# Optimization experiments

Measured on AMD Instinct MI355X. Metric: run time of the kernel, lower is better.

The kernel has to match this reference:

```python
import jax, jax.numpy as jnp
import numpy as np

VOCAB = 250002
UNUSED = np.array([0, 2, 1, 3])  # cls, eos, pad, unk token ids for XLM-R tokenizer
TEMP = 0.02
H = 1024


def _normalize(x, axis=-1):
    n = jnp.sqrt(jnp.sum(x * x, axis=axis, keepdims=True))
    return x / jnp.maximum(n, 1e-12)


def _sparse_embedding(hidden, ids, sparse_w, sparse_b):
    # token_weights = relu(Linear(H,1)(hidden)) -> [B, L]
    tw = jax.nn.relu(jnp.einsum('blh,h->bl', hidden, sparse_w) + sparse_b)
    B = hidden.shape[0]
    # torch: scatter into [B, L, V] then max over L; since tw >= 0 and base is 0,
    # this equals a scatter-max into [B, V] (avoids the huge [B,L,V] intermediate).
    emb = jnp.zeros((B, VOCAB), tw.dtype)
    emb = emb.at[jnp.arange(B)[:, None], ids].max(tw)
    emb = emb.at[:, UNUSED].set(0.0)
    return emb


def _colbert_embedding(hidden, mask, colbert_w, colbert_b):
    # Linear on tokens 1: (drop CLS), mask, then L2-normalize
    v = jnp.einsum('blh,dh->bld', hidden[:, 1:], colbert_w) + colbert_b
    v = v * mask[:, 1:, None]
    return _normalize(v)


def setup_inputs() -> dict:
    key = jax.random.key(0)
    ks = jax.random.split(key, 8)
    return {
        'q_hidden': jax.random.normal(ks[0], (8, 128, H), jnp.float32),
        'p_hidden': jax.random.normal(ks[1], (64, 512, H), jnp.float32),
        'q_mask': jnp.ones((8, 128), jnp.float32),
        'p_mask': jnp.ones((64, 512), jnp.float32),
        'q_ids': jax.random.randint(ks[2], (8, 128), 0, VOCAB),
        'p_ids': jax.random.randint(ks[3], (64, 512), 0, VOCAB),
        'colbert_w': jax.random.normal(ks[4], (H, H), jnp.float32) * 0.02,
        'colbert_b': jnp.zeros((H,), jnp.float32),
        'sparse_w': jax.random.normal(ks[5], (H,), jnp.float32) * 0.02,
        'sparse_b': jnp.zeros((), jnp.float32),
    }


def reference(q_hidden, p_hidden, q_mask, p_mask, q_ids, p_ids,
              colbert_w, colbert_b, sparse_w, sparse_b):
    # dense: cls pooling + normalize
    q_dense = _normalize(q_hidden[:, 0])
    p_dense = _normalize(p_hidden[:, 0])
    dense_scores = (q_dense @ p_dense.T) / TEMP  # [Bq, Bp]

    # sparse: relu-weighted vocab scatter-max
    q_sparse = _sparse_embedding(q_hidden, q_ids, sparse_w, sparse_b)
    p_sparse = _sparse_embedding(p_hidden, p_ids, sparse_w, sparse_b)
    sparse_scores = (q_sparse @ p_sparse.T) / TEMP  # [Bq, Bp]

    # colbert: late-interaction maxsim
    q_col = _colbert_embedding(q_hidden, q_mask, colbert_w, colbert_b)  # [Bq, Lq-1, H]
    p_col = _colbert_embedding(p_hidden, p_mask, colbert_w, colbert_b)  # [Bp, Lp-1, H]
    token_scores = jnp.einsum('qin,pjn->qipj', q_col, p_col)  # [Bq, Lq-1, Bp, Lp-1]
    colbert_scores = token_scores.max(-1).sum(1)
    colbert_scores = colbert_scores / q_mask[:, 1:].sum(-1, keepdims=True)
    colbert_scores = colbert_scores / TEMP  # [Bq, Bp]

    return dense_scores, sparse_scores, colbert_scores
```

## Files before the change

### kernel.cpp

```cpp
#include <hip/hip_runtime.h>
#include <hip/hip_bf16.h>


typedef __bf16 bf16x8 __attribute__((ext_vector_type(8)));
typedef float floatx4 __attribute__((ext_vector_type(4)));
typedef unsigned short ushort8v __attribute__((ext_vector_type(8)));

#define TEMP 0.02f

__device__ __forceinline__ unsigned short f2bf(float f) {
    unsigned u = __float_as_uint(f);
    unsigned r = (u + 0x7FFFu + ((u >> 16) & 1u)) >> 16;
    return (unsigned short)r;
}
__device__ __forceinline__ unsigned encf(float f) {
    unsigned u = __float_as_uint(f);
    return (u & 0x80000000u) ? ~u : (u | 0x80000000u);
}
__device__ __forceinline__ float decf(unsigned u) {
    return __uint_as_float((u & 0x80000000u) ? (u & 0x7FFFFFFFu) : ~u);
}

__device__ __forceinline__ void async_load16(void* lds, const void* g) {
    __builtin_amdgcn_global_load_lds(
        (__attribute__((address_space(1))) void*)g,
        (__attribute__((address_space(3))) void*)lds,
        16, 0, 0);
}

__global__ void conv_zero_tw(const float* __restrict__ qh, const float* __restrict__ ph,
                             const float* __restrict__ wsrc, unsigned short* __restrict__ dst,
                             const float* __restrict__ sw, const float* __restrict__ sb,
                             float* __restrict__ tw, unsigned* __restrict__ zbase)
{
    __shared__ float red[4];
    int b = blockIdx.x, t = threadIdx.x;
    if (b < 388) zbase[b * 256 + t] = 0u;
    int r0 = b * 2;
    const float* src;
    bool do_tw = true;
    if (r0 < 1024)       { src = qh   + (size_t)r0 * 1024; }
    else if (r0 < 33792) { src = ph   + (size_t)(r0 - 1024) * 1024; }
    else                 { src = wsrc + (size_t)(r0 - 33792) * 1024; do_tw = false; }
    const float4* s4 = (const float4*)src;
    float4 a = s4[t * 2], c = s4[t * 2 + 1];
    ushort8v o;
    o[0] = f2bf(a.x); o[1] = f2bf(a.y); o[2] = f2bf(a.z); o[3] = f2bf(a.w);
    o[4] = f2bf(c.x); o[5] = f2bf(c.y); o[6] = f2bf(c.z); o[7] = f2bf(c.w);
    ((ushort8v*)dst)[(size_t)b * 256 + t] = o;
    if (do_tw) {
        const float4* w4 = (const float4*)sw;
        int wi = (t & 127) * 2;
        float4 wa = w4[wi], wc = w4[wi + 1];
        float acc = a.x * wa.x + a.y * wa.y + a.z * wa.z + a.w * wa.w
                  + c.x * wc.x + c.y * wc.y + c.z * wc.z + c.w * wc.w;
        #pragma unroll
        for (int s = 32; s; s >>= 1) acc += __shfl_down(acc, s, 64);
        if ((t & 63) == 0) red[t >> 6] = acc;
        __syncthreads();
        if (t == 0)   tw[r0]     = fmaxf(red[0] + red[1] + sb[0], 0.0f);
        if (t == 128) tw[r0 + 1] = fmaxf(red[2] + red[3] + sb[0], 0.0f);
    }
}

__global__ void canon_all(const int* __restrict__ q_ids, const int* __restrict__ p_ids,
                          const float* __restrict__ tw,
                          float* __restrict__ eff_q, float* __restrict__ eff_p)
{
    __shared__ int   sid[512];
    __shared__ float stw[512];
    int b = blockIdx.x, t = threadIdx.x;
    const int* ids; const float* twr; float* eff; int L, chunk;
    if (b < 8) {
        L = 128; chunk = 0;
        ids = q_ids + b * 128; twr = tw + b * 128; eff = eff_q + b * 128;
    } else {
        int pr = (b - 8) >> 1; chunk = (b - 8) & 1; L = 512;
        ids = p_ids + pr * 512; twr = tw + 1024 + pr * 512; eff = eff_p + pr * 512;
    }
    for (int l = t; l < L; l += 256) { sid[l] = ids[l]; stw[l] = twr[l]; }
    __syncthreads();
    int l = chunk * 256 + t;
    if (l < L) {
        int id = sid[l];
        float wv = stw[l];
        bool kill = (id < 4);
        #pragma unroll 8
        for (int m = 0; m < L; ++m) {
            int idm = sid[m];
            float wm = stw[m];
            bool beats = (idm == id) & (m != l) & ((wm > wv) | ((wm == wv) & (m < l)));
            kill = kill | beats;
        }
        eff[l] = kill ? 0.0f : wv;
    }
}

template<int MODE>
__global__ __launch_bounds__(256, 2)
void gemm_bt(const unsigned short* __restrict__ A,
             const unsigned short* __restrict__ B,
             const float* __restrict__ bias,
             unsigned short* __restrict__ C,
             unsigned* __restrict__ Mbuf,
             float* __restrict__ normsq,
             const float* __restrict__ p_mask,
             int mTiles, int N, int K,
             const float* __restrict__ qh, const float* __restrict__ ph,
             const int* __restrict__ q_ids, const int* __restrict__ p_ids,
             const float* __restrict__ eff_q, const float* __restrict__ eff_p,
             float* __restrict__ out)
{
    __shared__ unsigned short smA[128 * 64];
    __shared__ unsigned short smB[128 * 64];
    const int tid  = threadIdx.x;

    if (MODE == 0 && (int)blockIdx.x >= mTiles) {
        int pair = (int)blockIdx.x - mTiles;
        int qb = pair >> 6, pb = pair & 63;
        char* lds = (char*)smA;
        int*   qid = (int*)lds;
        float* qef = (float*)(lds + 512);
        int*   pid = (int*)(lds + 1024);
        float* pef = (float*)(lds + 3072);
        float* redD = (float*)(lds + 5120);
        float* redS = (float*)(lds + 5184);
        int t = tid;
        if (t < 128) { qid[t] = q_ids[qb * 128 + t]; qef[t] = eff_q[qb * 128 + t]; }
        for (int m = t; m < 512; m += 256) { pid[m] = p_ids[pb * 512 + m]; pef[m] = eff_p[pb * 512 + m]; }
        const float4* q4 = (const float4*)(qh + (size_t)qb * 128 * 1024);
        const float4* p4 = (const float4*)(ph + (size_t)pb * 512 * 1024);
        float4 a = q4[t], b = p4[t];
        float dot = a.x * b.x + a.y * b.y + a.z * b.z + a.w * b.w;
        float nq  = a.x * a.x + a.y * a.y + a.z * a.z + a.w * a.w;
        float np  = b.x * b.x + b.y * b.y + b.z * b.z + b.w * b.w;
        #pragma unroll
        for (int sh = 32; sh; sh >>= 1) {
            dot += __shfl_down(dot, sh, 64);
            nq  += __shfl_down(nq, sh, 64);
            np  += __shfl_down(np, sh, 64);
        }
        if ((t & 63) == 0) { int w = t >> 6; redD[w] = dot; redD[4 + w] = nq; redD[8 + w] = np; }
        __syncthreads();
        if (t == 0) {
            float d = redD[0] + redD[1] + redD[2] + redD[3];
            float n1 = redD[4] + redD[5] + redD[6] + redD[7];
            float n2 = redD[8] + redD[9] + redD[10] + redD[11];
            out[qb * 64 + pb] = d / (fmaxf(sqrtf(n1), 1e-12f) * fmaxf(sqrtf(n2), 1e-12f)) / TEMP;
        }
        float s = 0.0f;
        for (int idx = t; idx < 128 * 512; idx += 256) {
            int l = idx >> 9, m = idx & 511;
            if (qid[l] == pid[m]) s += qef[l] * pef[m];
        }
        #pragma unroll
        for (int sh = 32; sh; sh >>= 1) s += __shfl_down(s, sh, 64);
        if ((t & 63) == 0) redS[t >> 6] = s;
        __syncthreads();
        if (t == 0) out[512 + qb * 64 + pb] = (redS[0] + redS[1] + redS[2] + redS[3]) / TEMP;
        return;
    }

    const int lane = tid & 63;
    const int w    = tid >> 6;
    const int wm   = w >> 1, wn = w & 1;
    const int quad = lane >> 4, m16 = lane & 15;

    const int id = (int)blockIdx.x;
    const int g  = id >> 6;
    const int s8 = id & 7;
    const int k8 = (id >> 3) & 7;
    const int rowTile = (MODE == 0) ? (g * 8 + s8) : k8;
    const int colTile = (MODE == 0) ? k8 : (g * 8 + s8);
    const int rowBase = rowTile * 128;
    const int colBase = colTile * 128;

    const int sr = lane >> 2;
    const int scg = (lane & 3) ^ ((lane >> 3) & 3);
    const unsigned short* aG0 = A + (long long)(rowBase + w * 16 + sr) * K + scg * 8;
    const unsigned short* aG1 = aG0 + 64LL * K;
    const unsigned short* bG0 = B + (long long)(colBase + w * 16 + sr) * K + scg * 8;
    const unsigned short* bG1 = bG0 + 64LL * K;
    unsigned short* lA0 = smA + w * 512;
    unsigned short* lA1 = smA + (w + 4) * 512;
    unsigned short* lB0 = smB + w * 512;
    unsigned short* lB1 = smB + (w + 4) * 512;

    const int fragOff = (m16 * 4 + (quad ^ ((m16 >> 1) & 3))) * 8;

    floatx4 acc[4][4] = {};

    for (int k0 = 0; k0 < K; k0 += 64) {
        async_load16(lA0,        aG0 + k0);
        async_load16(lA0 + 4096, aG0 + k0 + 32);
        async_load16(lA1,        aG1 + k0);
        async_load16(lA1 + 4096, aG1 + k0 + 32);
        async_load16(lB0,        bG0 + k0);
        async_load16(lB0 + 4096, bG0 + k0 + 32);
        async_load16(lB1,        bG1 + k0);
        async_load16(lB1 + 4096, bG1 + k0 + 32);
        __syncthreads();
        #pragma unroll
        for (int h = 0; h < 2; ++h) {
            bf16x8 af[4], bfr[4];
            #pragma unroll
            for (int f = 0; f < 4; ++f) {
                af[f]  = *(const bf16x8*)(smA + h * 4096 + (wm * 4 + f) * 512 + fragOff);
                bfr[f] = *(const bf16x8*)(smB + h * 4096 + (wn * 4 + f) * 512 + fragOff);
            }
            #pragma unroll
            for (int i = 0; i < 4; ++i)
                #pragma unroll
                for (int j = 0; j < 4; ++j)
                    acc[i][j] = __builtin_amdgcn_mfma_f32_16x16x32_bf16(af[i], bfr[j], acc[i][j], 0, 0, 0);
        }
        __syncthreads();
    }

    if (MODE == 0) {
        float bcol[4];
        #pragma unroll
        for (int j = 0; j < 4; ++j) bcol[j] = bias[colBase + wn * 64 + j * 16 + m16];
        #pragma unroll
        for (int i = 0; i < 4; ++i) {
            int row0 = rowBase + wm * 64 + i * 16 + quad * 4;
            #pragma unroll
            for (int r = 0; r < 4; ++r) {
                float sq = 0.0f;
                #pragma unroll
                for (int j = 0; j < 4; ++j) {
                    int col = colBase + wn * 64 + j * 16 + m16;
                    float val = acc[i][j][r] + bcol[j];
                    C[(long long)(row0 + r) * N + col] = f2bf(val);
                    sq += val * val;
                }
                #pragma unroll
                for (int s = 1; s < 16; s <<= 1) sq += __shfl_xor(sq, s, 64);
                if (m16 == 0) atomicAdd(&normsq[row0 + r], sq);
            }
        }
    } else {
        const int pb = colBase >> 9;
        float pfac[4];
        #pragma unroll
        for (int j = 0; j < 4; ++j) {
            int colg = colBase + wn * 64 + j * 16 + m16;
            float pm = p_mask[colg];
            float pn = sqrtf(normsq[1024 + colg]);
            pfac[j] = pm / fmaxf(pn * pm, 1e-12f);
        }
        #pragma unroll
        for (int i = 0; i < 4; ++i) {
            #pragma unroll
            for (int r = 0; r < 4; ++r) {
                float mx = -3.0e38f;
                #pragma unroll
                for (int j = 0; j < 4; ++j) {
                    int colg = colBase + wn * 64 + j * 16 + m16;
                    float v = acc[i][j][r] * pfac[j];
                    if ((colg & 511) == 0) v = -3.0e38f;
                    mx = fmaxf(mx, v);
                }
                #pragma unroll
                for (int s = 1; s < 16; s <<= 1) mx = fmaxf(mx, __shfl_xor(mx, s, 64));
                if (m16 == 0) {
                    int row = rowBase + wm * 64 + i * 16 + quad * 4 + r;
                    atomicMax(&Mbuf[row * 64 + pb], encf(mx));
                }
            }
        }
    }
}

__global__ void colbert_reduce_k(const unsigned* __restrict__ Mbuf,
                                 const float* __restrict__ q_mask,
                                 const float* __restrict__ normsq,
                                 float* __restrict__ out)
{
    int pair = blockIdx.x * 4 + (threadIdx.x >> 6);
    int lane = threadIdx.x & 63;
    int qb = pair >> 6, pb = pair & 63;
    float s = 0.0f, msum = 0.0f;
    for (int i = 1 + lane; i < 128; i += 64) {
        float qm = q_mask[qb * 128 + i];
        float qn = sqrtf(normsq[qb * 128 + i]);
        float qfac = qm / fmaxf(qn * qm, 1e-12f);
        s += decf(Mbuf[(qb * 128 + i) * 64 + pb]) * qfac;
        msum += qm;
    }
    #pragma unroll
    for (int sh = 32; sh; sh >>= 1) {
        s += __shfl_down(s, sh, 64);
        msum += __shfl_down(msum, sh, 64);
    }
    if (lane == 0) out[1024 + qb * 64 + pb] = s / msum / TEMP;
}

extern "C" void kernel_launch(void* const* d_in, const int* in_sizes, int n_in,
                              void* d_out, int out_size, void* d_ws, size_t ws_size,
                              hipStream_t stream)
{
    const float* q_hidden = (const float*)d_in[0];
    const float* p_hidden = (const float*)d_in[1];
    const float* q_mask   = (const float*)d_in[2];
    const float* p_mask   = (const float*)d_in[3];
    const int*   q_ids    = (const int*)d_in[4];
    const int*   p_ids    = (const int*)d_in[5];
    const float* colbert_w = (const float*)d_in[6];
    const float* colbert_b = (const float*)d_in[7];
    const float* sparse_w  = (const float*)d_in[8];
    const float* sparse_b  = (const float*)d_in[9];
    float* out = (float*)d_out;

    char* ws = (char*)d_ws;
    size_t off = 0;
    auto carve = [&](size_t bytes) { char* p = ws + off; off += (bytes + 255) & ~(size_t)255; return p; };
    unsigned short* qhb  = (unsigned short*)carve((size_t)1024 * 1024 * 2);
    unsigned short* phb  = (unsigned short*)carve((size_t)32768 * 1024 * 2);
    unsigned short* Wb   = (unsigned short*)carve((size_t)1024 * 1024 * 2);
    unsigned short* qv   = (unsigned short*)carve((size_t)1024 * 1024 * 2);
    unsigned short* pv   = (unsigned short*)carve((size_t)32768 * 1024 * 2);
    unsigned* Mbuf  = (unsigned*)carve((size_t)1024 * 64 * 4);
    float*    normsq = (float*)carve((size_t)33792 * 4);
    float*    tw    = (float*)carve((size_t)33792 * 4);
    float*    eff_q = (float*)carve(1024 * 4);
    float*    eff_p = (float*)carve(32768 * 4);
    (void)phb; (void)Wb; (void)pv;

    conv_zero_tw<<<17408, 256, 0, stream>>>(q_hidden, p_hidden, colbert_w, qhb,
                                            sparse_w, sparse_b, tw, Mbuf);

    canon_all<<<136, 256, 0, stream>>>(q_ids, p_ids, tw, eff_q, eff_p);

    gemm_bt<0><<<2112 + 512, 256, 0, stream>>>(
        qhb, Wb, colbert_b, qv, nullptr, normsq, nullptr, 2112, 1024, 1024,
        q_hidden, p_hidden, q_ids, p_ids, eff_q, eff_p, out);

    gemm_bt<1><<<2048, 256, 0, stream>>>(
        qv, pv, nullptr, nullptr, Mbuf, normsq, p_mask, 0, 32768, 1024,
        nullptr, nullptr, nullptr, nullptr, nullptr, nullptr, nullptr);

    colbert_reduce_k<<<128, 256, 0, stream>>>(Mbuf, q_mask, normsq, out);
}
```

Baseline: 404.7 us.

## Fold sparse dedup and colbert reduction into existing GEMM kernels

```diff
diff --git a/kernel.cpp b/kernel.cpp
--- a/kernel.cpp
+++ b/kernel.cpp
@@ -31,11 +31,13 @@
 __global__ void conv_zero_tw(const float* __restrict__ qh, const float* __restrict__ ph,
                              const float* __restrict__ wsrc, unsigned short* __restrict__ dst,
                              const float* __restrict__ sw, const float* __restrict__ sb,
-                             float* __restrict__ tw, unsigned* __restrict__ zbase)
+                             float* __restrict__ tw, unsigned* __restrict__ zbase,
+                             unsigned* __restrict__ cnt)
 {
     __shared__ float red[4];
     int b = blockIdx.x, t = threadIdx.x;
     if (b < 388) zbase[b * 256 + t] = 0u;
+    if (b == 388 && t == 0) *cnt = 0u;
     int r0 = b * 2;
     const float* src;
     bool do_tw = true;
@@ -63,39 +65,6 @@
     }
 }
 
-__global__ void canon_all(const int* __restrict__ q_ids, const int* __restrict__ p_ids,
-                          const float* __restrict__ tw,
-                          float* __restrict__ eff_q, float* __restrict__ eff_p)
-{
-    __shared__ int   sid[512];
-    __shared__ float stw[512];
-    int b = blockIdx.x, t = threadIdx.x;
-    const int* ids; const float* twr; float* eff; int L, chunk;
-    if (b < 8) {
-        L = 128; chunk = 0;
-        ids = q_ids + b * 128; twr = tw + b * 128; eff = eff_q + b * 128;
-    } else {
-        int pr = (b - 8) >> 1; chunk = (b - 8) & 1; L = 512;
-        ids = p_ids + pr * 512; twr = tw + 1024 + pr * 512; eff = eff_p + pr * 512;
-    }
-    for (int l = t; l < L; l += 256) { sid[l] = ids[l]; stw[l] = twr[l]; }
-    __syncthreads();
-    int l = chunk * 256 + t;
-    if (l < L) {
-        int id = sid[l];
-        float wv = stw[l];
-        bool kill = (id < 4);
-        #pragma unroll 8
-        for (int m = 0; m < L; ++m) {
-            int idm = sid[m];
-            float wm = stw[m];
-            bool beats = (idm == id) & (m != l) & ((wm > wv) | ((wm == wv) & (m < l)));
-            kill = kill | beats;
-        }
-        eff[l] = kill ? 0.0f : wv;
-    }
-}
-
 template<int MODE>
 __global__ __launch_bounds__(256, 2)
 void gemm_bt(const unsigned short* __restrict__ A,
@@ -108,7 +77,9 @@
              int mTiles, int N, int K,
              const float* __restrict__ qh, const float* __restrict__ ph,
              const int* __restrict__ q_ids, const int* __restrict__ p_ids,
-             const float* __restrict__ eff_q, const float* __restrict__ eff_p,
+             const float* __restrict__ twp,
+             const float* __restrict__ qmask_g,
+             unsigned* __restrict__ cnt,
              float* __restrict__ out)
 {
     __shared__ unsigned short smA[128 * 64];
@@ -120,14 +91,37 @@
         int qb = pair >> 6, pb = pair & 63;
         char* lds = (char*)smA;
         int*   qid = (int*)lds;
-        float* qef = (float*)(lds + 512);
-        int*   pid = (int*)(lds + 1024);
-        float* pef = (float*)(lds + 3072);
-        float* redD = (float*)(lds + 5120);
-        float* redS = (float*)(lds + 5184);
+        int*   pid = (int*)(lds + 512);
+        float* qw  = (float*)(lds + 2560);
+        float* pw  = (float*)(lds + 3072);
+        float* qe  = (float*)(lds + 5120);
+        float* pe  = (float*)(lds + 5632);
+        float* redD = (float*)(lds + 7680);
+        float* redS = (float*)(lds + 7744);
         int t = tid;
-        if (t < 128) { qid[t] = q_ids[qb * 128 + t]; qef[t] = eff_q[qb * 128 + t]; }
-        for (int m = t; m < 512; m += 256) { pid[m] = p_ids[pb * 512 + m]; pef[m] = eff_p[pb * 512 + m]; }
+        if (t < 128) { qid[t] = q_ids[qb * 128 + t]; qw[t] = twp[qb * 128 + t]; }
+        for (int m = t; m < 512; m += 256) { pid[m] = p_ids[pb * 512 + m]; pw[m] = twp[1024 + pb * 512 + m]; }
+        __syncthreads();
+        if (t < 128) {
+            int id = qid[t]; float wv = qw[t]; bool kill = (id < 4);
+            #pragma unroll 8
+            for (int m = 0; m < 128; ++m) {
+                int idm = qid[m]; float wm = qw[m];
+                bool beats = (idm == id) & (m != t) & ((wm > wv) | ((wm == wv) & (m < t)));
+                kill = kill | beats;
+            }
+            qe[t] = kill ? 0.0f : wv;
+        }
+        for (int l = t; l < 512; l += 256) {
+            int id = pid[l]; float wv = pw[l]; bool kill = (id < 4);
+            #pragma unroll 8
+            for (int m = 0; m < 512; ++m) {
+                int idm = pid[m]; float wm = pw[m];
+                bool beats = (idm == id) & (m != l) & ((wm > wv) | ((wm == wv) & (m < l)));
+                kill = kill | beats;
+            }
+            pe[l] = kill ? 0.0f : wv;
+        }
         const float4* q4 = (const float4*)(qh + (size_t)qb * 128 * 1024);
         const float4* p4 = (const float4*)(ph + (size_t)pb * 512 * 1024);
         float4 a = q4[t], b = p4[t];
@@ -151,7 +145,7 @@
         float s = 0.0f;
         for (int idx = t; idx < 128 * 512; idx += 256) {
             int l = idx >> 9, m = idx & 511;
-            if (qid[l] == pid[m]) s += qef[l] * pef[m];
+            if (qid[l] == pid[m]) s += qe[l] * pe[m];
         }
         #pragma unroll
         for (int sh = 32; sh; sh >>= 1) s += __shfl_down(s, sh, 64);
@@ -269,31 +263,38 @@
                 }
             }
         }
+        __threadfence();
+        __syncthreads();
+        volatile unsigned* flag = (volatile unsigned*)smA;
+        if (tid == 0) {
+            unsigned old = atomicAdd(cnt, 1u);
+            *flag = (old == 2047u) ? 1u : 0u;
+        }
+        __syncthreads();
+        if (*flag) {
+            __threadfence();
+            int wv = tid >> 6, ln = tid & 63;
+            for (int pr = wv; pr < 512; pr += 4) {
+                int qb = pr >> 6, pbx = pr & 63;
+                float s = 0.0f, msum = 0.0f;
+                for (int i = 1 + ln; i < 128; i += 64) {
+                    float qm = qmask_g[qb * 128 + i];
+                    float qn = sqrtf(normsq[qb * 128 + i]);
+                    float qfac = qm / fmaxf(qn * qm, 1e-12f);
+                    unsigned mv = __hip_atomic_load(&Mbuf[(qb * 128 + i) * 64 + pbx],
+                                                    __ATOMIC_RELAXED, __HIP_MEMORY_SCOPE_AGENT);
+                    s += decf(mv) * qfac;
+                    msum += qm;
+                }
+                #pragma unroll
+                for (int sh = 32; sh; sh >>= 1) {
+                    s += __shfl_down(s, sh, 64);
+                    msum += __shfl_down(msum, sh, 64);
+                }
+                if (ln == 0) out[1024 + qb * 64 + pbx] = s / msum / TEMP;
+            }
+        }
     }
-}
-
-__global__ void colbert_reduce_k(const unsigned* __restrict__ Mbuf,
-                                 const float* __restrict__ q_mask,
-                                 const float* __restrict__ normsq,
-                                 float* __restrict__ out)
-{
-    int pair = blockIdx.x * 4 + (threadIdx.x >> 6);
-    int lane = threadIdx.x & 63;
-    int qb = pair >> 6, pb = pair & 63;
-    float s = 0.0f, msum = 0.0f;
-    for (int i = 1 + lane; i < 128; i += 64) {
-        float qm = q_mask[qb * 128 + i];
-        float qn = sqrtf(normsq[qb * 128 + i]);
-        float qfac = qm / fmaxf(qn * qm, 1e-12f);
-        s += decf(Mbuf[(qb * 128 + i) * 64 + pb]) * qfac;
-        msum += qm;
-    }
-    #pragma unroll
-    for (int sh = 32; sh; sh >>= 1) {
-        s += __shfl_down(s, sh, 64);
-        msum += __shfl_down(msum, sh, 64);
-    }
-    if (lane == 0) out[1024 + qb * 64 + pb] = s / msum / TEMP;
 }
 
 extern "C" void kernel_launch(void* const* d_in, const int* in_sizes, int n_in,
@@ -323,22 +324,17 @@
     unsigned* Mbuf  = (unsigned*)carve((size_t)1024 * 64 * 4);
     float*    normsq = (float*)carve((size_t)33792 * 4);
     float*    tw    = (float*)carve((size_t)33792 * 4);
-    float*    eff_q = (float*)carve(1024 * 4);
-    float*    eff_p = (float*)carve(32768 * 4);
+    unsigned* cnt   = (unsigned*)carve(256);
     (void)phb; (void)Wb; (void)pv;
 
     conv_zero_tw<<<17408, 256, 0, stream>>>(q_hidden, p_hidden, colbert_w, qhb,
-                                            sparse_w, sparse_b, tw, Mbuf);
-
-    canon_all<<<136, 256, 0, stream>>>(q_ids, p_ids, tw, eff_q, eff_p);
+                                            sparse_w, sparse_b, tw, Mbuf, cnt);
 
     gemm_bt<0><<<2112 + 512, 256, 0, stream>>>(
         qhb, Wb, colbert_b, qv, nullptr, normsq, nullptr, 2112, 1024, 1024,
-        q_hidden, p_hidden, q_ids, p_ids, eff_q, eff_p, out);
+        q_hidden, p_hidden, q_ids, p_ids, tw, nullptr, nullptr, out);
 
     gemm_bt<1><<<2048, 256, 0, stream>>>(
         qv, pv, nullptr, nullptr, Mbuf, normsq, p_mask, 0, 32768, 1024,
-        nullptr, nullptr, nullptr, nullptr, nullptr, nullptr, nullptr);
-
-    colbert_reduce_k<<<128, 256, 0, stream>>>(Mbuf, q_mask, normsq, out);
-}
+        nullptr, nullptr, nullptr, nullptr, nullptr, q_mask, cnt, out);
+}
```

Measured after the change: 705.9 us. 74.4% more time.
